# Kernel optimization log

Hardware: AMD Instinct MI355X
Metric: run time of the kernel (lower is better)

Reference implementation:

```python
import jax, jax.numpy as jnp
import numpy as np


def _scinol_new_p(p0, S2, G, eta, M, cond):
    # SCINOL effective-parameter computation (done under no_grad in torch)
    denom = jnp.sqrt(S2 + M * M)
    theta = jnp.clip(G / denom, -1.0, 1.0)
    upd = jnp.where(cond, theta / (2.0 * denom) * eta, 0.0)
    return p0 + jax.lax.stop_gradient(upd)


def _conv(x, w, b):
    y = jax.lax.conv_general_dilated(x, w, window_strides=(1, 1), padding='VALID',
                                     dimension_numbers=('NCHW', 'OIHW', 'NCHW'))
    return y + b[None, :, None, None]


def _maxpool2(x):
    return jax.lax.reduce_window(x, -jnp.inf, jax.lax.max, (1, 1, 2, 2), (1, 1, 2, 2), 'VALID')


def _scinol_conv(x, w0, wS2, wG, weta, wM, b0, bS2, bG, beta):
    # M-update: per-input-channel mean (over batch) of max-abs over H,W
    stat = jax.lax.stop_gradient(jnp.mean(jnp.max(jnp.abs(x), axis=(2, 3)), axis=0))  # (C_in,)
    M = jnp.maximum(stat, wM)  # (C_in,)
    w = _scinol_new_p(w0, wS2, wG, weta, M[None, :, None, None], wG != 0)
    b = _scinol_new_p(b0, bS2, bG, beta, jnp.float32(1.0), bG != 0)
    return _conv(x, w, b)


def _scinol_linear(x, w0, wS2, wG, weta, wM, b0, bS2, bG, beta):
    stat = jax.lax.stop_gradient(jnp.mean(jnp.abs(x), axis=0))  # (in_features,)
    M = jnp.maximum(wM, stat)  # broadcast -> (out, in)
    w = _scinol_new_p(w0, wS2, wG, weta, M, wS2 != 0)
    b = _scinol_new_p(b0, bS2, bG, beta, jnp.float32(1.0), bS2 != 0)
    return x @ w.T + b


def setup_inputs() -> dict:
    key = jax.random.key(0)
    ks = iter(jax.random.split(key, 40))
    f32 = jnp.float32
    d = {}
    d['x'] = jax.random.normal(next(ks), (2048, 1, 28, 28), dtype=f32)
    for pre, wshape, cin in [('c1', (64, 1, 5, 5), 1), ('c2', (64, 64, 5, 5), 64)]:
        d[pre + '_w0'] = jax.random.normal(next(ks), wshape, dtype=f32) * 0.1
        d[pre + '_wS2'] = jax.random.uniform(next(ks), wshape, dtype=f32)
        d[pre + '_wG'] = jax.random.normal(next(ks), wshape, dtype=f32)
        d[pre + '_weta'] = jax.random.uniform(next(ks), wshape, dtype=f32)
        d[pre + '_wM'] = jax.random.uniform(next(ks), (cin,), dtype=f32)
        d[pre + '_b0'] = jax.random.normal(next(ks), (64,), dtype=f32) * 0.1
        d[pre + '_bS2'] = jax.random.uniform(next(ks), (64,), dtype=f32)
        d[pre + '_bG'] = jax.random.normal(next(ks), (64,), dtype=f32)
        d[pre + '_beta'] = jax.random.uniform(next(ks), (64,), dtype=f32)
    d['l_w0'] = jax.random.normal(next(ks), (10, 1024), dtype=f32) * 0.03
    d['l_wS2'] = jax.random.uniform(next(ks), (10, 1024), dtype=f32)
    d['l_wG'] = jax.random.normal(next(ks), (10, 1024), dtype=f32)
    d['l_weta'] = jax.random.uniform(next(ks), (10, 1024), dtype=f32)
    d['l_wM'] = jax.random.uniform(next(ks), (10, 1024), dtype=f32)
    d['l_b0'] = jax.random.normal(next(ks), (10,), dtype=f32) * 0.03
    d['l_bS2'] = jax.random.uniform(next(ks), (10,), dtype=f32)
    d['l_bG'] = jax.random.normal(next(ks), (10,), dtype=f32)
    d['l_beta'] = jax.random.uniform(next(ks), (10,), dtype=f32)
    return d


def reference(x,
              c1_w0, c1_wS2, c1_wG, c1_weta, c1_wM, c1_b0, c1_bS2, c1_bG, c1_beta,
              c2_w0, c2_wS2, c2_wG, c2_weta, c2_wM, c2_b0, c2_bS2, c2_bG, c2_beta,
              l_w0, l_wS2, l_wG, l_weta, l_wM, l_b0, l_bS2, l_bG, l_beta):
    h = _scinol_conv(x, c1_w0, c1_wS2, c1_wG, c1_weta, c1_wM, c1_b0, c1_bS2, c1_bG, c1_beta)
    h = _maxpool2(jax.nn.relu(h))                      # (N,64,12,12)
    h = _scinol_conv(h, c2_w0, c2_wS2, c2_wG, c2_weta, c2_wM, c2_b0, c2_bS2, c2_bG, c2_beta)
    h = _maxpool2(jax.nn.relu(h))                      # (N,64,4,4)
    h = h.reshape(h.shape[0], -1)                      # (N,1024)
    return _scinol_linear(h, l_w0, l_wS2, l_wG, l_weta, l_wM, l_b0, l_bS2, l_bG, l_beta)
```

## Files before the change

### kernel.cpp

```cpp
#include <hip/hip_runtime.h>
#include <hip/hip_bf16.h>

typedef float v4f __attribute__((ext_vector_type(4)));
typedef short v8s __attribute__((ext_vector_type(8)));

#define WS_STAT2   0
#define WS_STATL   64
#define WS_B1      1088
#define WS_B2      1152
#define WS_WL      1216
#define WS_BL      11456
#define WS_IMAX    11520
#define WS_W1F_B   54272
#define WS_WP2_B   62464
#define WS_P1_B    267264
#define WS_P2_B    38016000
#define WS_C1MAX_F 9504000
#define WS_LPART_F 66816

__global__ void k_stat1(const float* __restrict__ x, float* ws) {
    int tid = threadIdx.x;
    int wv = tid >> 6, lane = tid & 63;
    int n = blockIdx.x * 4 + wv;
    const float* p = x + n * 784;
    float m = 0.f;
    for (int i = lane; i < 784; i += 64) m = fmaxf(m, fabsf(p[i]));
#pragma unroll
    for (int off = 32; off; off >>= 1) m = fmaxf(m, __shfl_xor(m, off, 64));
    if (lane == 0) ws[WS_IMAX + n] = m;
}

__global__ void k_prepw1(const float* __restrict__ w0, const float* __restrict__ S2,
                         const float* __restrict__ G, const float* __restrict__ eta,
                         const float* __restrict__ wM,
                         const float* __restrict__ b0, const float* __restrict__ bS2,
                         const float* __restrict__ bG, const float* __restrict__ beta,
                         float* ws) {
    __shared__ float red[256];
    int tid = threadIdx.x;
    float p = 0.f;
    for (int i = tid; i < 2048; i += 256) p += ws[WS_IMAX + i];
    red[tid] = p;
    __syncthreads();
    for (int s = 128; s > 0; s >>= 1) {
        if (tid < s) red[tid] += red[tid + s];
        __syncthreads();
    }
    float M = fmaxf(red[0] * (1.f / 2048.f), wM[0]);

    int i = blockIdx.x * 256 + tid;
    if (i < 4096) {
        int j = i & 7, m16 = (i >> 3) & 15, q = (i >> 7) & 3, ot = i >> 9;
        int tap = q * 8 + j, oc = m16 * 4 + ot;
        float v = 0.f;
        if (tap < 25) {
            int s = oc * 25 + tap;
            float g = G[s];
            float den = sqrtf(S2[s] + M * M);
            float inv = 1.f / den;
            float th = fminf(fmaxf(g * inv, -1.f), 1.f);
            v = w0[s] + ((g != 0.f) ? th * 0.5f * inv * eta[s] : 0.f);
        }
        ((__hip_bfloat16*)((char*)ws + WS_W1F_B))[i] = __float2bfloat16(v);
    } else if (i < 4160) {
        int c = i - 4096;
        float g = bG[c];
        float den = sqrtf(bS2[c] + 1.f);
        float inv = 1.f / den;
        float th = fminf(fmaxf(g * inv, -1.f), 1.f);
        ws[WS_B1 + c] = b0[c] + ((g != 0.f) ? th * 0.5f * inv * beta[c] : 0.f);
    }
}

__global__ void __launch_bounds__(256)
k_conv1(const float* __restrict__ x, float* ws, __hip_bfloat16* __restrict__ pool1) {
    __shared__ __align__(16) float sX[1024];
    __shared__ int sMax[64];
    int n = blockIdx.x, tid = threadIdx.x;
    int wv = tid >> 6, lane = tid & 63;
    int m16 = lane & 15, quad = lane >> 4;

    {
        const float4* src = (const float4*)(x + (size_t)n * 784);
        float4 v = {0.f, 0.f, 0.f, 0.f};
        if (tid < 196) v = src[tid];
        ((float4*)sX)[tid] = v;
    }
    if (tid < 64) sMax[tid] = 0;

    const ushort* wfrag = (const ushort*)((const char*)ws + WS_W1F_B);
    v8s bfr[4];
#pragma unroll
    for (int ot = 0; ot < 4; ++ot)
        bfr[ot] = *(const v8s*)(wfrag + ((ot * 4 + quad) * 16 + m16) * 8);
    float4 bias = *(const float4*)(ws + WS_B1 + m16 * 4);

    int dj[8];
#pragma unroll
    for (int j = 0; j < 8; ++j) {
        int tap = quad * 8 + j;
        int u = (tap * 13) >> 6;
        dj[j] = tap + 23 * u;
    }

    int W0 = wv * 36 + (m16 >> 2);
    int wy = (W0 * 171) >> 11;
    int wx = W0 - wy * 12;
    int coff = 28 * ((m16 >> 1) & 1) + (m16 & 1);

    __syncthreads();

    float vmax[4] = {0.f, 0.f, 0.f, 0.f};
    ushort* op = (ushort*)(pool1 + (size_t)n * 9216);

    float g[8];
    {
        int base = 56 * wy + 2 * wx + coff;
#pragma unroll
        for (int j = 0; j < 8; ++j) g[j] = sX[base + dj[j]];
    }
    for (int mt = 0; mt < 9; ++mt) {
        union { v8s v; ushort us[8]; } ua;
#pragma unroll
        for (int j = 0; j < 8; ++j)
            ua.us[j] = __bfloat16_as_ushort(__float2bfloat16(g[j]));

        wx += 4;
        if (wx >= 12) { wx -= 12; ++wy; }
        if (mt < 8) {
            int nb = 56 * wy + 2 * wx + coff;
#pragma unroll
            for (int j = 0; j < 8; ++j) g[j] = sX[nb + dj[j]];
        }

        v4f z = {0.f, 0.f, 0.f, 0.f};
        v4f acc[4];
#pragma unroll
        for (int ot = 0; ot < 4; ++ot)
            acc[ot] = __builtin_amdgcn_mfma_f32_16x16x32_bf16(ua.v, bfr[ot], z, 0, 0, 0);

        int Wd = (wv * 9 + mt) * 4 + quad;
        ushort4 pk;
#pragma unroll
        for (int ot = 0; ot < 4; ++ot) {
            v4f a = acc[ot];
            float m = fmaxf(fmaxf(a[0], a[1]), fmaxf(a[2], a[3]));
            float pv = fmaxf(m + bias[ot], 0.f);
            vmax[ot] = fmaxf(vmax[ot], pv);
            ((ushort*)&pk)[ot] = __bfloat16_as_ushort(__float2bfloat16(pv));
        }
        *(ushort4*)(op + Wd * 64 + m16 * 4) = pk;
    }

#pragma unroll
    for (int ot = 0; ot < 4; ++ot) {
        float m = vmax[ot];
        m = fmaxf(m, __shfl_xor(m, 16, 64));
        m = fmaxf(m, __shfl_xor(m, 32, 64));
        if (lane < 16) atomicMax(&sMax[lane * 4 + ot], __float_as_int(m));
    }
    __syncthreads();
    if (tid < 64) ws[WS_C1MAX_F + n * 64 + tid] = __int_as_float(sMax[tid]);
}

__global__ void k_stat2red(float* ws) {
    __shared__ float red[256];
    int c = blockIdx.x, t = threadIdx.x;
    float s = 0.f;
    for (int n = t; n < 2048; n += 256) s += ws[WS_C1MAX_F + n * 64 + c];
    red[t] = s;
    __syncthreads();
    for (int k = 128; k > 0; k >>= 1) {
        if (t < k) red[t] += red[t + k];
        __syncthreads();
    }
    if (t == 0) ws[WS_STAT2 + c] = red[0] * (1.f / 2048.f);
}

__global__ void k_prepw2(const float* __restrict__ w0, const float* __restrict__ S2,
                         const float* __restrict__ G, const float* __restrict__ eta,
                         const float* __restrict__ wM,
                         const float* __restrict__ b0, const float* __restrict__ bS2,
                         const float* __restrict__ bG, const float* __restrict__ beta,
                         float* ws, __hip_bfloat16* __restrict__ wp2) {
    int i = blockIdx.x * 256 + threadIdx.x;
    int j = i & 7, m16 = (i >> 3) & 15, quad = (i >> 7) & 3;
    int ot = (i >> 9) & 3, kc = (i >> 11) & 1, uv = i >> 12;
    int oc = ot * 16 + m16, ic = kc * 32 + quad * 8 + j;
    int s = oc * 1600 + ic * 25 + uv;
    float M = fmaxf(ws[WS_STAT2 + ic], wM[ic]);
    float g = G[s];
    float den = sqrtf(S2[s] + M * M);
    float inv = 1.f / den;
    float th = fminf(fmaxf(g * inv, -1.f), 1.f);
    float v = w0[s] + ((g != 0.f) ? th * 0.5f * inv * eta[s] : 0.f);
    wp2[i] = __float2bfloat16(v);
    if (blockIdx.x == 0 && threadIdx.x < 64) {
        int c = threadIdx.x;
        float gb = bG[c];
        float den2 = sqrtf(bS2[c] + 1.f);
        float inv2 = 1.f / den2;
        float th2 = fminf(fmaxf(gb * inv2, -1.f), 1.f);
        ws[WS_B2 + c] = b0[c] + ((gb != 0.f) ? th2 * 0.5f * inv2 * beta[c] : 0.f);
    }
}

__global__ void __launch_bounds__(128)
k_conv2(const ushort* __restrict__ pool1, const ushort* __restrict__ wp2,
        const float* __restrict__ ws, float* __restrict__ pool2) {
    __shared__ __align__(16) ushort sImg[2 * 10368];
    int tid = threadIdx.x;
    int wv = tid >> 6, lane = tid & 63;
    int n0 = blockIdx.x * 2;

    {
        const uint4* src = (const uint4*)(pool1 + (size_t)n0 * 9216);
        uint4* dst = (uint4*)sImg;
#pragma unroll
        for (int i = 0; i < 18; ++i) {
            int c = tid + i * 128;
            dst[(c >> 3) * 9 + (c & 7)] = src[c];
        }
    }

    int m16 = lane & 15, quad = lane >> 4;
    int q8 = quad * 8;
    int x0 = m16 & 7;
    int yb = m16 >> 3;
    v4f acc[4][4];
#pragma unroll
    for (int i = 0; i < 4; ++i)
#pragma unroll
        for (int j = 0; j < 4; ++j) acc[i][j] = (v4f){0.f, 0.f, 0.f, 0.f};

    const ushort* wlane = wp2 + lane * 8;
    v8s bf[2][2][4];
#pragma unroll
    for (int kc = 0; kc < 2; ++kc)
#pragma unroll
        for (int ot = 0; ot < 4; ++ot)
            bf[0][kc][ot] = *(const v8s*)(wlane + (kc * 4 + ot) * 512);

    __syncthreads();

    const ushort* simg = sImg + wv * 10368;
#pragma unroll
    for (int uvIdx = 0; uvIdx < 25; ++uvIdx) {
        int cur = uvIdx & 1, nxt = cur ^ 1;
        if (uvIdx < 24) {
            const ushort* wnext = wlane + (uvIdx + 1) * 4096;
#pragma unroll
            for (int kc = 0; kc < 2; ++kc)
#pragma unroll
                for (int ot = 0; ot < 4; ++ot)
                    bf[nxt][kc][ot] = *(const v8s*)(wnext + (kc * 4 + ot) * 512);
        }
        int u = (uvIdx * 13) >> 6;
        int v = uvIdx - u * 5;
        v8s a[2][4];
#pragma unroll
        for (int kc = 0; kc < 2; ++kc)
#pragma unroll
            for (int pt = 0; pt < 4; ++pt)
                a[kc][pt] = *(const v8s*)(simg +
                    ((pt * 2 + yb + u) * 12 + x0 + v) * 72 + kc * 32 + q8);
#pragma unroll
        for (int kc = 0; kc < 2; ++kc)
#pragma unroll
            for (int pt = 0; pt < 4; ++pt)
#pragma unroll
                for (int ot = 0; ot < 4; ++ot)
                    acc[pt][ot] = __builtin_amdgcn_mfma_f32_16x16x32_bf16(
                        a[kc][pt], bf[cur][kc][ot], acc[pt][ot], 0, 0, 0);
    }

    int n = n0 + wv;
    float bv[4];
#pragma unroll
    for (int ot = 0; ot < 4; ++ot) bv[ot] = ws[WS_B2 + ot * 16 + m16];
    float* outp = pool2 + (size_t)n * 1024;
#pragma unroll
    for (int pt = 0; pt < 4; ++pt)
#pragma unroll
        for (int ot = 0; ot < 4; ++ot) {
            v4f a = acc[pt][ot];
            float m01 = fmaxf(a[0], a[1]);
            float m23 = fmaxf(a[2], a[3]);
            m01 = fmaxf(m01, __shfl_xor(m01, 32, 64));
            m23 = fmaxf(m23, __shfl_xor(m23, 32, 64));
            if (lane < 32) {
                int oc = ot * 16 + m16;
                int f = oc * 16 + pt * 4 + (quad & 1) * 2;
                outp[f] = fmaxf(m01 + bv[ot], 0.f);
                outp[f + 1] = fmaxf(m23 + bv[ot], 0.f);
            }
        }
}

__global__ void k_statl(const float* __restrict__ pool2, float* ws) {
    int b = blockIdx.x, tid = threadIdx.x;
    float4 s = {0.f, 0.f, 0.f, 0.f};
    for (int im = 0; im < 32; ++im) {
        float4 v = ((const float4*)(pool2 + (size_t)(b * 32 + im) * 1024))[tid];
        s.x += v.x; s.y += v.y; s.z += v.z; s.w += v.w;
    }
    ((float4*)(ws + WS_LPART_F + b * 1024))[tid] = s;
}

__global__ void k_prepwl(const float* __restrict__ w0, const float* __restrict__ S2,
                         const float* __restrict__ G, const float* __restrict__ eta,
                         const float* __restrict__ wM,
                         const float* __restrict__ b0, const float* __restrict__ bS2,
                         const float* __restrict__ bG, const float* __restrict__ beta,
                         float* ws) {
    int i = blockIdx.x * 256 + threadIdx.x;
    if (i < 10240) {
        int f = i & 1023;
        float s = 0.f;
#pragma unroll
        for (int b = 0; b < 64; ++b) s += ws[WS_LPART_F + b * 1024 + f];
        float stat = s * (1.f / 2048.f);
        float M = fmaxf(wM[i], stat);
        float s2 = S2[i];
        float den = sqrtf(s2 + M * M);
        float inv = 1.f / den;
        float th = fminf(fmaxf(G[i] * inv, -1.f), 1.f);
        ws[WS_WL + i] = w0[i] + ((s2 != 0.f) ? th * 0.5f * inv * eta[i] : 0.f);
    } else if (i < 10250) {
        int c = i - 10240;
        float s2 = bS2[c];
        float den = sqrtf(s2 + 1.f);
        float inv = 1.f / den;
        float th = fminf(fmaxf(bG[c] * inv, -1.f), 1.f);
        ws[WS_BL + c] = b0[c] + ((s2 != 0.f) ? th * 0.5f * inv * beta[c] : 0.f);
    }
}

__global__ void k_linear(const float* __restrict__ pool2, const float* __restrict__ ws,
                         float* __restrict__ out) {
    int tid = threadIdx.x;
    int wv = tid >> 6, lane = tid & 63;
    int n = blockIdx.x * 4 + wv;
    const float* hp = pool2 + (size_t)n * 1024;
    float h[16];
#pragma unroll
    for (int j = 0; j < 16; ++j) h[j] = hp[j * 64 + lane];
    for (int oc = 0; oc < 10; ++oc) {
        const float* wp = ws + WS_WL + oc * 1024;
        float d = 0.f;
#pragma unroll
        for (int j = 0; j < 16; ++j) d = fmaf(h[j], wp[j * 64 + lane], d);
#pragma unroll
        for (int off = 32; off; off >>= 1) d += __shfl_xor(d, off, 64);
        if (lane == 0) out[n * 10 + oc] = d + ws[WS_BL + oc];
    }
}

extern "C" void kernel_launch(void* const* d_in, const int* in_sizes, int n_in,
                              void* d_out, int out_size, void* d_ws, size_t ws_size,
                              hipStream_t stream) {
    const float* x = (const float*)d_in[0];
    float* ws = (float*)d_ws;
    __hip_bfloat16* wp2 = (__hip_bfloat16*)((char*)d_ws + WS_WP2_B);
    __hip_bfloat16* p1 = (__hip_bfloat16*)((char*)d_ws + WS_P1_B);
    float* p2 = (float*)((char*)d_ws + WS_P2_B);
    float* out = (float*)d_out;

    k_stat1<<<512, 256, 0, stream>>>(x, ws);
    k_prepw1<<<17, 256, 0, stream>>>(
        (const float*)d_in[1], (const float*)d_in[2], (const float*)d_in[3],
        (const float*)d_in[4], (const float*)d_in[5], (const float*)d_in[6],
        (const float*)d_in[7], (const float*)d_in[8], (const float*)d_in[9], ws);
    k_conv1<<<2048, 256, 0, stream>>>(x, ws, p1);
    k_stat2red<<<64, 256, 0, stream>>>(ws);
    k_prepw2<<<400, 256, 0, stream>>>(
        (const float*)d_in[10], (const float*)d_in[11], (const float*)d_in[12],
        (const float*)d_in[13], (const float*)d_in[14], (const float*)d_in[15],
        (const float*)d_in[16], (const float*)d_in[17], (const float*)d_in[18], ws, wp2);
    k_conv2<<<1024, 128, 0, stream>>>((const ushort*)p1, (const ushort*)wp2, ws, p2);
    k_statl<<<64, 256, 0, stream>>>(p2, ws);
    k_prepwl<<<41, 256, 0, stream>>>(
        (const float*)d_in[19], (const float*)d_in[20], (const float*)d_in[21],
        (const float*)d_in[22], (const float*)d_in[23], (const float*)d_in[24],
        (const float*)d_in[25], (const float*)d_in[26], (const float*)d_in[27], ws);
    k_linear<<<512, 256, 0, stream>>>(p2, ws, out);
}
```

Before: 210.5 us.

## Split conv2 output channels across two waves per image and XOR-swizzle LDS

The conv2 kernel now launches 256 threads per block, with two waves per image, each computing half of the 64 output channels. This halves the accumulator and weight-register footprint per wave so more waves can be resident. The LDS image layout drops the padded 72-element row stride in favour of a dense 64-element row with an XOR swizzle on the 16-byte chunk index, which cuts shared memory per block and is meant to avoid bank conflicts. In exchange, each image tile is now read from LDS by two waves, and the weight fetches are split between them.

```diff
diff --git a/kernel.cpp b/kernel.cpp
--- a/kernel.cpp
+++ b/kernel.cpp
@@ -205,10 +205,10 @@
     }
 }
 
-__global__ void __launch_bounds__(128)
+__global__ void __launch_bounds__(256, 3)
 k_conv2(const ushort* __restrict__ pool1, const ushort* __restrict__ wp2,
         const float* __restrict__ ws, float* __restrict__ pool2) {
-    __shared__ __align__(16) ushort sImg[2 * 10368];
+    __shared__ __align__(16) ushort sImg[2 * 9216];
     int tid = threadIdx.x;
     int wv = tid >> 6, lane = tid & 63;
     int n0 = blockIdx.x * 2;
@@ -217,33 +217,38 @@
         const uint4* src = (const uint4*)(pool1 + (size_t)n0 * 9216);
         uint4* dst = (uint4*)sImg;
 #pragma unroll
-        for (int i = 0; i < 18; ++i) {
-            int c = tid + i * 128;
-            dst[(c >> 3) * 9 + (c & 7)] = src[c];
+        for (int i = 0; i < 9; ++i) {
+            int c = tid + i * 256;
+            int r = c >> 3, col = c & 7;
+            dst[r * 8 + (col ^ (r & 7))] = src[c];
         }
     }
 
     int m16 = lane & 15, quad = lane >> 4;
-    int q8 = quad * 8;
+    int img = wv >> 1, oth = wv & 1;
     int x0 = m16 & 7;
     int yb = m16 >> 3;
-    v4f acc[4][4];
+    int rbase = yb * 12 + x0;
+
+    v4f acc[4][2];
 #pragma unroll
     for (int i = 0; i < 4; ++i)
 #pragma unroll
-        for (int j = 0; j < 4; ++j) acc[i][j] = (v4f){0.f, 0.f, 0.f, 0.f};
-
-    const ushort* wlane = wp2 + lane * 8;
-    v8s bf[2][2][4];
+        for (int j = 0; j < 2; ++j) acc[i][j] = (v4f){0.f, 0.f, 0.f, 0.f};
+
+    const ushort* wlane = wp2 + oth * 1024 + lane * 8;
+    v8s bf[2][2][2];
 #pragma unroll
     for (int kc = 0; kc < 2; ++kc)
 #pragma unroll
-        for (int ot = 0; ot < 4; ++ot)
-            bf[0][kc][ot] = *(const v8s*)(wlane + (kc * 4 + ot) * 512);
-
-    __syncthreads();
-
-    const ushort* simg = sImg + wv * 10368;
+        for (int o2 = 0; o2 < 2; ++o2)
+            bf[0][kc][o2] = *(const v8s*)(wlane + (kc * 4 + o2) * 512);
+
+    __syncthreads();
+
+    const ushort* simg = sImg + img * 9216;
+    int ck0 = quad;
+    int ck1 = 4 + quad;
 #pragma unroll
     for (int uvIdx = 0; uvIdx < 25; ++uvIdx) {
         int cur = uvIdx & 1, nxt = cur ^ 1;
@@ -252,47 +257,49 @@
 #pragma unroll
             for (int kc = 0; kc < 2; ++kc)
 #pragma unroll
-                for (int ot = 0; ot < 4; ++ot)
-                    bf[nxt][kc][ot] = *(const v8s*)(wnext + (kc * 4 + ot) * 512);
+                for (int o2 = 0; o2 < 2; ++o2)
+                    bf[nxt][kc][o2] = *(const v8s*)(wnext + (kc * 4 + o2) * 512);
         }
         int u = (uvIdx * 13) >> 6;
         int v = uvIdx - u * 5;
+        int r0 = rbase + u * 12 + v;
         v8s a[2][4];
 #pragma unroll
+        for (int pt = 0; pt < 4; ++pt) {
+            int row = r0 + pt * 24;
+            int rs = row & 7;
+            a[0][pt] = *(const v8s*)(simg + row * 64 + ((ck0 ^ rs) << 3));
+            a[1][pt] = *(const v8s*)(simg + row * 64 + ((ck1 ^ rs) << 3));
+        }
+#pragma unroll
         for (int kc = 0; kc < 2; ++kc)
 #pragma unroll
             for (int pt = 0; pt < 4; ++pt)
-                a[kc][pt] = *(const v8s*)(simg +
-                    ((pt * 2 + yb + u) * 12 + x0 + v) * 72 + kc * 32 + q8);
-#pragma unroll
-        for (int kc = 0; kc < 2; ++kc)
-#pragma unroll
-            for (int pt = 0; pt < 4; ++pt)
-#pragma unroll
-                for (int ot = 0; ot < 4; ++ot)
-                    acc[pt][ot] = __builtin_amdgcn_mfma_f32_16x16x32_bf16(
-                        a[kc][pt], bf[cur][kc][ot], acc[pt][ot], 0, 0, 0);
-    }
-
-    int n = n0 + wv;
-    float bv[4];
-#pragma unroll
-    for (int ot = 0; ot < 4; ++ot) bv[ot] = ws[WS_B2 + ot * 16 + m16];
+#pragma unroll
+                for (int o2 = 0; o2 < 2; ++o2)
+                    acc[pt][o2] = __builtin_amdgcn_mfma_f32_16x16x32_bf16(
+                        a[kc][pt], bf[cur][kc][o2], acc[pt][o2], 0, 0, 0);
+    }
+
+    int n = n0 + img;
+    float bv[2];
+#pragma unroll
+    for (int o2 = 0; o2 < 2; ++o2) bv[o2] = ws[WS_B2 + (oth * 2 + o2) * 16 + m16];
     float* outp = pool2 + (size_t)n * 1024;
 #pragma unroll
     for (int pt = 0; pt < 4; ++pt)
 #pragma unroll
-        for (int ot = 0; ot < 4; ++ot) {
-            v4f a = acc[pt][ot];
+        for (int o2 = 0; o2 < 2; ++o2) {
+            v4f a = acc[pt][o2];
             float m01 = fmaxf(a[0], a[1]);
             float m23 = fmaxf(a[2], a[3]);
             m01 = fmaxf(m01, __shfl_xor(m01, 32, 64));
             m23 = fmaxf(m23, __shfl_xor(m23, 32, 64));
             if (lane < 32) {
-                int oc = ot * 16 + m16;
+                int oc = (oth * 2 + o2) * 16 + m16;
                 int f = oc * 16 + pt * 4 + (quad & 1) * 2;
-                outp[f] = fmaxf(m01 + bv[ot], 0.f);
-                outp[f + 1] = fmaxf(m23 + bv[ot], 0.f);
+                outp[f] = fmaxf(m01 + bv[o2], 0.f);
+                outp[f + 1] = fmaxf(m23 + bv[o2], 0.f);
             }
         }
 }
@@ -377,7 +384,7 @@
         (const float*)d_in[10], (const float*)d_in[11], (const float*)d_in[12],
         (const float*)d_in[13], (const float*)d_in[14], (const float*)d_in[15],
         (const float*)d_in[16], (const float*)d_in[17], (const float*)d_in[18], ws, wp2);
-    k_conv2<<<1024, 128, 0, stream>>>((const ushort*)p1, (const ushort*)wp2, ws, p2);
+    k_conv2<<<1024, 256, 0, stream>>>((const ushort*)p1, (const ushort*)wp2, ws, p2);
     k_statl<<<64, 256, 0, stream>>>(p2, ws);
     k_prepwl<<<41, 256, 0, stream>>>(
         (const float*)d_in[19], (const float*)d_in[20], (const float*)d_in[21],
```

New measurement: 200.6 us. 4.7% less time.
